# Kernel optimization log

Measured on AMD Instinct MI355X. Metric: run time of the kernel, lower is better.

Reference implementation:

```python
import jax, jax.numpy as jnp
import numpy as np

N_HEADS = 16
NEG_BIG = float(-2**32 + 1)  # value the original writes into masked positions


def setup_inputs() -> dict:
    key = jax.random.key(0)
    ks = jax.random.split(key, 5)
    B, T, D = 64, 256, 1024
    s = 1.0 / np.sqrt(D)
    return {
        "x": jax.random.normal(ks[0], (B, T, D), jnp.float32),
        "pos_emb": jax.random.normal(ks[1], (T, D), jnp.float32),
        "Wq": jax.random.normal(ks[2], (D, D), jnp.float32) * s,
        "Wk": jax.random.normal(ks[3], (D, D), jnp.float32) * s,
        "Wv": jax.random.normal(ks[4], (D, D), jnp.float32) * s,
    }


def reference(x, pos_emb, Wq, Wk, Wv):
    B, T, D = x.shape
    H = N_HEADS
    dh = D // H
    # add position embeddings (same arange positions for every batch row)
    temporal = x + pos_emb[None, :T, :]            # [B, T, D]
    q = temporal @ Wq                              # [B, T, D]
    k = temporal @ Wk
    v = temporal @ Wv
    # chunk along feature dim into H heads, concatenate along batch dim -> [H*B, T, dh]
    def split_heads(t):
        return jnp.concatenate(jnp.split(t, H, axis=2), axis=0)
    q_, k_, v_ = split_heads(q), split_heads(k), split_heads(v)
    scores = jnp.einsum('btd,bsd->bts', q_, k_) / jnp.sqrt(jnp.asarray(T, x.dtype))  # [H*B, T, T]
    # original masks the LOWER triangle (tril > 0 -> padding), faithful to source
    tril = jnp.tril(jnp.ones((T, T), x.dtype))
    scores = jnp.where(tril > 0, jnp.asarray(NEG_BIG, x.dtype), scores)
    # original applies softmax over dim=0 (the batch*head axis), faithful to source
    probs = jax.nn.softmax(scores, axis=0)         # [H*B, T, T]
    out = jnp.einsum('bts,bsd->btd', probs, v_)    # [H*B, T, dh]
    # merge heads back: chunk along batch dim, concatenate along feature dim
    out = jnp.concatenate(jnp.split(out, H, axis=0), axis=-1)  # [B, T, D]
    return out
```

## Files before the change

### kernel.cpp

```cpp
#include <hip/hip_runtime.h>

constexpr int SEQ = 256;
constexpr int DIM = 1024;
constexpr float SCALE = 0.0625f;

typedef __attribute__((ext_vector_type(8))) short bf16x8;
typedef __attribute__((ext_vector_type(4))) float f32x4;
typedef unsigned short ushort_t;
typedef unsigned int uint_t;

__device__ __forceinline__ void gld_lds16(const void* g, void* l) {
  __builtin_amdgcn_global_load_lds(
      (const __attribute__((address_space(1))) unsigned int*)g,
      (__attribute__((address_space(3))) unsigned int*)l, 16, 0, 0);
}

__device__ __forceinline__ ushort_t f2bf(float f) {
  uint_t u = __float_as_uint(f);
  return (ushort_t)((u + 0x7fffu + ((u >> 16) & 1u)) >> 16);
}

__global__ __launch_bounds__(256)
void prep_a(const float* __restrict__ x, const float* __restrict__ pos,
            ushort_t* __restrict__ Ab) {
  const size_t idx = ((size_t)blockIdx.x * 256 + threadIdx.x) * 8;
  const int m = (int)(idx >> 10), k = (int)(idx & 1023);
  float4 x0 = *(const float4*)(x + idx);
  float4 x1 = *(const float4*)(x + idx + 4);
  const float* pp = pos + ((size_t)(m & 255) << 10) + k;
  float4 p0 = *(const float4*)pp;
  float4 p1 = *(const float4*)(pp + 4);
  uint_t w0 = (uint_t)f2bf(x0.x + p0.x) | ((uint_t)f2bf(x0.y + p0.y) << 16);
  uint_t w1 = (uint_t)f2bf(x0.z + p0.z) | ((uint_t)f2bf(x0.w + p0.w) << 16);
  uint_t w2 = (uint_t)f2bf(x1.x + p1.x) | ((uint_t)f2bf(x1.y + p1.y) << 16);
  uint_t w3 = (uint_t)f2bf(x1.z + p1.z) | ((uint_t)f2bf(x1.w + p1.w) << 16);
  *(uint4*)&Ab[idx] = make_uint4(w0, w1, w2, w3);
}

__global__ __launch_bounds__(256)
void pack_w(const float* __restrict__ Wq, const float* __restrict__ Wk,
            const float* __restrict__ Wv, ushort_t* __restrict__ Bp) {
  const float* W = (blockIdx.z == 0) ? Wq : (blockIdx.z == 1) ? Wk : Wv;
  const int n  = blockIdx.x * 256 + threadIdx.x;
  const int k8 = blockIdx.y * 8;
  uint_t h[8];
#pragma unroll
  for (int i = 0; i < 8; ++i) h[i] = f2bf(W[(size_t)(k8 + i) * DIM + n]);
  uint_t hp[4];
#pragma unroll
  for (int j = 0; j < 4; ++j) hp[j] = h[2 * j] | (h[2 * j + 1] << 16);
  const int np = blockIdx.z * 1024 + n;
  const int nb = np >> 7, nl = np & 127;
  const int kc = k8 >> 6, kk = k8 & 63;
  size_t base = (((size_t)nb * 16 + kc) * 128 + nl) * 64 + kk;
  *(uint4*)&Bp[base] = make_uint4(hp[0], hp[1], hp[2], hp[3]);
}

__global__ __launch_bounds__(256)
void qkv_mfma(const ushort_t* __restrict__ Ab, const ushort_t* __restrict__ Bp,
              ushort_t* __restrict__ q_bf, ushort_t* __restrict__ k_bf,
              ushort_t* __restrict__ vT_bf) {
  const int nb = blockIdx.x;
  const int mb = blockIdx.y;
  const int tid = threadIdx.x;
  const int wave = tid >> 6, lane = tid & 63;
  const int wm = wave & 1, wn = wave >> 1;
  const int l15 = lane & 15, quad = lane >> 4;

  __shared__ ushort_t smem[18432];
  ushort_t* As = smem;
  ushort_t* Bs = smem + 8192;

  f32x4 acc[4][4] = {};

  const int sr = lane >> 3;
  const int scg = (lane & 7) ^ (sr & 7);
  const size_t arow = ((size_t)mb * 128 + wave * 32 + sr) * 1024;
  const size_t btile0 = ((size_t)nb * 16) * 128 * 64;

  const int swz = l15 & 7;
  const int a_off0 = (wm * 64 + l15) * 64 + ((quad) ^ swz) * 8;
  const int a_off1 = (wm * 64 + l15) * 64 + ((4 + quad) ^ swz) * 8;
  const int b_off0 = (wn * 64 + l15) * 64 + ((quad) ^ swz) * 8;
  const int b_off1 = (wn * 64 + l15) * 64 + ((4 + quad) ^ swz) * 8;

  for (int kc = 0; kc < 16; ++kc) {
    __syncthreads();
#pragma unroll
    for (int c = 0; c < 4; ++c)
      gld_lds16(Ab + arow + (size_t)c * 8192 + kc * 64 + scg * 8,
                &As[(wave * 32 + c * 8) * 64]);
    const ushort_t* bt = Bp + btile0 + (size_t)kc * 8192;
#pragma unroll
    for (int c = 0; c < 4; ++c)
      gld_lds16(bt + (wave * 32 + c * 8 + sr) * 64 + scg * 8,
                &Bs[(wave * 32 + c * 8) * 64]);
    __syncthreads();

    bf16x8 a0[4], a1[4], b0[4], b1[4];
#pragma unroll
    for (int i = 0; i < 4; ++i) {
      a0[i] = *(const bf16x8*)&As[a_off0 + i * 1024];
      a1[i] = *(const bf16x8*)&As[a_off1 + i * 1024];
    }
#pragma unroll
    for (int j = 0; j < 4; ++j) {
      b0[j] = *(const bf16x8*)&Bs[b_off0 + j * 1024];
      b1[j] = *(const bf16x8*)&Bs[b_off1 + j * 1024];
    }
#pragma unroll
    for (int i = 0; i < 4; ++i)
#pragma unroll
      for (int j = 0; j < 4; ++j) {
        acc[i][j] = __builtin_amdgcn_mfma_f32_16x16x32_bf16(a0[i], b0[j], acc[i][j], 0, 0, 0);
        acc[i][j] = __builtin_amdgcn_mfma_f32_16x16x32_bf16(a1[i], b1[j], acc[i][j], 0, 0, 0);
      }
  }

  const int wq = nb >> 3;
  const int h  = (nb & 7) * 2 + wn;
  const int b  = mb >> 1;
  const int tb0 = (mb & 1) * 128 + wm * 64;
  if (wq < 2) {
    ushort_t* base = ((wq == 0) ? q_bf : k_bf) + (size_t)(b * 16 + h) * SEQ * 64;
    const int tb = tb0 + quad * 4;
#pragma unroll
    for (int i = 0; i < 4; ++i)
#pragma unroll
      for (int j = 0; j < 4; ++j) {
        const int d = l15 + j * 16;
#pragma unroll
        for (int r = 0; r < 4; ++r)
          base[(size_t)(tb + i * 16 + r) * 64 + d] = f2bf(acc[i][j][r]);
      }
  } else {
    __syncthreads();
    ushort_t* L = smem + wave * (64 * 72);
#pragma unroll
    for (int i = 0; i < 4; ++i)
#pragma unroll
      for (int j = 0; j < 4; ++j) {
        uint_t lo = (uint_t)f2bf(acc[i][j][0]) | ((uint_t)f2bf(acc[i][j][1]) << 16);
        uint_t hi = (uint_t)f2bf(acc[i][j][2]) | ((uint_t)f2bf(acc[i][j][3]) << 16);
        *(uint2*)&L[(l15 + j * 16) * 72 + i * 16 + quad * 4] = make_uint2(lo, hi);
      }
    ushort_t* vbase = vT_bf + (size_t)(b * 16 + h) * 64 * SEQ + tb0;
    const int dr = lane >> 3;
    const int tc = (lane & 7) * 8;
#pragma unroll
    for (int u = 0; u < 8; ++u) {
      const int d = u * 8 + dr;
      uint4 val = *(const uint4*)&L[d * 72 + tc];
      *(uint4*)&vbase[(size_t)d * SEQ + tc] = val;
    }
  }
}

__global__ __launch_bounds__(256)
void stats_mfma(const ushort_t* __restrict__ qb, const ushort_t* __restrict__ kb,
                float* __restrict__ part_l) {
  const int p = blockIdx.x, g = blockIdx.y;
  int tt, ss;
  if (p < 4) { tt = p; ss = p; }
  else {
    const int idx = p - 4;
    tt = (idx < 3) ? 0 : (idx < 5) ? 1 : 2;
    ss = (idx < 3) ? idx + 1 : (idx < 5) ? idx - 1 : 3;
  }
  const bool diag = (p < 4);
  const int tid = threadIdx.x, wave = tid >> 6, lane = tid & 63;
  const int l15 = lane & 15, quad = lane >> 4;
  const int slot = g * 4 + wave;

  f32x4 lacc[4][4] = {};

  for (int i4 = 0; i4 < 4; ++i4) {
    const int bp = slot * 4 + i4;
    const int bh = (bp & 63) * 16 + (bp >> 6);
    const ushort_t* qt = qb + (size_t)bh * (SEQ * 64) + (size_t)(tt * 64) * 64;
    const ushort_t* kt = kb + (size_t)bh * (SEQ * 64) + (size_t)(ss * 64) * 64;
    bf16x8 aq[4][2], bk[4][2];
#pragma unroll
    for (int m = 0; m < 4; ++m)
#pragma unroll
      for (int ks = 0; ks < 2; ++ks) {
        aq[m][ks] = *(const bf16x8*)&qt[(m * 16 + l15) * 64 + ks * 32 + quad * 8];
        bk[m][ks] = *(const bf16x8*)&kt[(m * 16 + l15) * 64 + ks * 32 + quad * 8];
      }
    f32x4 sf[4][4] = {};
#pragma unroll
    for (int ks = 0; ks < 2; ++ks)
#pragma unroll
      for (int m = 0; m < 4; ++m)
#pragma unroll
        for (int n = 0; n < 4; ++n)
          sf[m][n] = __builtin_amdgcn_mfma_f32_16x16x32_bf16(aq[m][ks], bk[n][ks], sf[m][n], 0, 0, 0);
#pragma unroll
    for (int m = 0; m < 4; ++m)
#pragma unroll
      for (int n = 0; n < 4; ++n)
#pragma unroll
        for (int r = 0; r < 4; ++r) {
          float e = __expf(sf[m][n][r] * SCALE);
          if (diag) {
            const int t = tt * 64 + m * 16 + quad * 4 + r;
            const int s = ss * 64 + n * 16 + l15;
            e = (s > t) ? e : 1.0f;
          }
          lacc[m][n][r] += e;
        }
  }
  float* pl = part_l + (size_t)slot * (SEQ * SEQ);
#pragma unroll
  for (int m = 0; m < 4; ++m)
#pragma unroll
    for (int r = 0; r < 4; ++r) {
      const int t = tt * 64 + m * 16 + quad * 4 + r;
#pragma unroll
      for (int n = 0; n < 4; ++n)
        pl[(size_t)t * SEQ + ss * 64 + n * 16 + l15] = lacc[m][n][r];
    }
}

__global__ __launch_bounds__(256)
void merge_kernel(const float* __restrict__ part_l, float* __restrict__ inv_lT) {
  const int i = blockIdx.x * 256 + threadIdx.x;
  const int t = i >> 8, s = i & 255;
  float invv;
  if (s <= t) invv = 1.0f / 1024.0f;
  else {
    float sum = 0.f;
    for (int g = 0; g < 256; ++g) sum += part_l[(size_t)g * (SEQ * SEQ) + i];
    invv = 1.0f / sum;
  }
  inv_lT[s * SEQ + t] = invv;
}

__global__ __launch_bounds__(256)
void pv_mfma(const ushort_t* __restrict__ qb, const ushort_t* __restrict__ kb,
             const ushort_t* __restrict__ vtb, const float* __restrict__ inv_lT,
             float* __restrict__ out) {
  const int bh = blockIdx.x;
  const int b = bh >> 4, h = bh & 15;
  const int tid = threadIdx.x, wave = tid >> 6, lane = tid & 63;
  const int l15 = lane & 15, quad = lane >> 4;
  const int t0 = wave * 64;

  __shared__ ushort_t Plds[4][64][72];
  ushort_t (*Pw)[72] = Plds[wave];

  const ushort_t* qq = qb + (size_t)bh * (SEQ * 64);
  const ushort_t* kk = kb + (size_t)bh * (SEQ * 64);
  const ushort_t* vv = vtb + (size_t)bh * (64 * SEQ);

  bf16x8 qf[4][2];
#pragma unroll
  for (int nt = 0; nt < 4; ++nt)
#pragma unroll
    for (int ks = 0; ks < 2; ++ks)
      qf[nt][ks] = *(const bf16x8*)&qq[(t0 + nt * 16 + l15) * 64 + ks * 32 + quad * 8];

  f32x4 o[4][4] = {};

  for (int sc = 0; sc < 4; ++sc) {
    if (sc < wave) {
      const uint_t c = 0x3A803A80u;
      const uint4 cc = make_uint4(c, c, c, c);
#pragma unroll
      for (int u = 0; u < 8; ++u) *(uint4*)&Pw[lane][u * 8] = cc;
    } else {
      bf16x8 kf[4][2];
#pragma unroll
      for (int ms = 0; ms < 4; ++ms)
#pragma unroll
        for (int ks = 0; ks < 2; ++ks)
          kf[ms][ks] = *(const bf16x8*)&kk[(sc * 64 + ms * 16 + l15) * 64 + ks * 32 + quad * 8];
      f32x4 sf[4][4] = {};
#pragma unroll
      for (int ks = 0; ks < 2; ++ks)
#pragma unroll
        for (int ms = 0; ms < 4; ++ms)
#pragma unroll
          for (int nt = 0; nt < 4; ++nt)
            sf[ms][nt] = __builtin_amdgcn_mfma_f32_16x16x32_bf16(kf[ms][ks], qf[nt][ks], sf[ms][nt], 0, 0, 0);
      const bool dg = (sc == wave);
      const int t = t0 + l15;
#pragma unroll
      for (int ms = 0; ms < 4; ++ms)
#pragma unroll
        for (int nt = 0; nt < 4; ++nt) {
          const int sb = sc * 64 + ms * 16 + quad * 4;
          const int tc = t + nt * 16;
          ushort_t pb[4];
#pragma unroll
          for (int r = 0; r < 4; ++r) {
            const int s = sb + r;
            float e = __expf(sf[ms][nt][r] * SCALE);
            if (dg) e = (s > tc) ? e : 1.0f;
            pb[r] = f2bf(e * inv_lT[(size_t)s * SEQ + tc]);
          }
          uint_t lo = (uint_t)pb[0] | ((uint_t)pb[1] << 16);
          uint_t hi = (uint_t)pb[2] | ((uint_t)pb[3] << 16);
          *(uint2*)&Pw[nt * 16 + l15][ms * 16 + quad * 4] = make_uint2(lo, hi);
        }
    }
    bf16x8 vf[4][2], pf[4][2];
#pragma unroll
    for (int nd = 0; nd < 4; ++nd)
#pragma unroll
      for (int ks = 0; ks < 2; ++ks)
        vf[nd][ks] = *(const bf16x8*)&vv[(nd * 16 + l15) * SEQ + sc * 64 + ks * 32 + quad * 8];
#pragma unroll
    for (int mt = 0; mt < 4; ++mt)
#pragma unroll
      for (int ks = 0; ks < 2; ++ks)
        pf[mt][ks] = *(const bf16x8*)&Pw[mt * 16 + l15][ks * 32 + quad * 8];
#pragma unroll
    for (int ks = 0; ks < 2; ++ks)
#pragma unroll
      for (int mt = 0; mt < 4; ++mt)
#pragma unroll
        for (int nd = 0; nd < 4; ++nd)
          o[mt][nd] = __builtin_amdgcn_mfma_f32_16x16x32_bf16(pf[mt][ks], vf[nd][ks], o[mt][nd], 0, 0, 0);
  }

  float* ob = out + (size_t)b * SEQ * DIM + h * 64;
#pragma unroll
  for (int mt = 0; mt < 4; ++mt)
#pragma unroll
    for (int r = 0; r < 4; ++r) {
      const int t = t0 + mt * 16 + quad * 4 + r;
#pragma unroll
      for (int nd = 0; nd < 4; ++nd)
        ob[(size_t)t * DIM + nd * 16 + l15] = o[mt][nd][r];
    }
}

extern "C" void kernel_launch(void* const* d_in, const int* in_sizes, int n_in,
                              void* d_out, int out_size, void* d_ws, size_t ws_size,
                              hipStream_t stream) {
  const float* x   = (const float*)d_in[0];
  const float* pos = (const float*)d_in[1];
  const float* Wq  = (const float*)d_in[2];
  const float* Wk  = (const float*)d_in[3];
  const float* Wv  = (const float*)d_in[4];
  float* out = (float*)d_out;

  ushort_t* Ab = (ushort_t*)d_out;
  ushort_t* Bp = (ushort_t*)((char*)d_out + 33554432);

  char* W = (char*)d_ws;
  ushort_t* q_bf   = (ushort_t*)(W);
  ushort_t* k_bf   = (ushort_t*)(W + 33554432);
  ushort_t* vT_bf  = (ushort_t*)(W + 67108864);
  float*    part_l = (float*)  (W + 100663296);
  float*    inv_lT = (float*)  (W + 167772160);

  prep_a<<<dim3(8192), 256, 0, stream>>>(x, pos, Ab);
  pack_w<<<dim3(4, 128, 3), 256, 0, stream>>>(Wq, Wk, Wv, Bp);
  qkv_mfma<<<dim3(24, 128), 256, 0, stream>>>(Ab, Bp, q_bf, k_bf, vT_bf);
  stats_mfma<<<dim3(10, 64), 256, 0, stream>>>(q_bf, k_bf, part_l);
  merge_kernel<<<dim3(SEQ * SEQ / 256), 256, 0, stream>>>(part_l, inv_lT);
  pv_mfma<<<dim3(1024), 256, 0, stream>>>(q_bf, k_bf, vT_bf, inv_lT, out);
}
```

Before: 374.9 us.

## Enlarge QKV GEMM tiles to 256x256 with double-buffered LDS pipeline

The QKV projection GEMM moves from 128x128 tiles with 4 waves to 256x256 tiles with 8 waves. The K-loop is now software-pipelined, with two LDS buffers, staged global-to-LDS loads interleaved with MFMA phases, explicit vmcnt waits and setprio. The weight packing layout changes to match the 256-wide N tiles. The aim is more data reuse per tile and hiding of load latency behind MFMAs. Separately, the merge kernel's 256-way reduction is split across 8 independent accumulators to raise memory-level parallelism. The risks are higher register pressure and 128KB of LDS per block, which limits occupancy.

```diff
diff --git a/kernel.cpp b/kernel.cpp
--- a/kernel.cpp
+++ b/kernel.cpp
@@ -50,110 +50,141 @@
 #pragma unroll
   for (int j = 0; j < 4; ++j) hp[j] = h[2 * j] | (h[2 * j + 1] << 16);
   const int np = blockIdx.z * 1024 + n;
-  const int nb = np >> 7, nl = np & 127;
+  const int nb = np >> 8, nl = np & 255;
   const int kc = k8 >> 6, kk = k8 & 63;
-  size_t base = (((size_t)nb * 16 + kc) * 128 + nl) * 64 + kk;
+  size_t base = (((size_t)nb * 16 + kc) * 256 + nl) * 64 + kk;
   *(uint4*)&Bp[base] = make_uint4(hp[0], hp[1], hp[2], hp[3]);
 }
 
-__global__ __launch_bounds__(256)
+__global__ __launch_bounds__(512, 2)
 void qkv_mfma(const ushort_t* __restrict__ Ab, const ushort_t* __restrict__ Bp,
               ushort_t* __restrict__ q_bf, ushort_t* __restrict__ k_bf,
               ushort_t* __restrict__ vT_bf) {
   const int nb = blockIdx.x;
   const int mb = blockIdx.y;
-  const int tid = threadIdx.x;
+  const int tid = (int)threadIdx.x;
   const int wave = tid >> 6, lane = tid & 63;
-  const int wm = wave & 1, wn = wave >> 1;
+  const int wm = wave >> 2, wn = wave & 3;
   const int l15 = lane & 15, quad = lane >> 4;
 
-  __shared__ ushort_t smem[18432];
-  ushort_t* As = smem;
-  ushort_t* Bs = smem + 8192;
-
-  f32x4 acc[4][4] = {};
-
-  const int sr = lane >> 3;
-  const int scg = (lane & 7) ^ (sr & 7);
-  const size_t arow = ((size_t)mb * 128 + wave * 32 + sr) * 1024;
-  const size_t btile0 = ((size_t)nb * 16) * 128 * 64;
+  __shared__ ushort_t smem[65536];
+
+  const int r8 = lane >> 3;
+  const int lc8 = ((lane & 7) ^ r8) * 8;
+  const size_t a_row = ((size_t)(mb * 256 + wave * 8 + r8)) << 10;
+  const size_t b_row = ((size_t)((nb * 16) * 256 + wave * 8 + r8)) << 6;
+  const int wb = wave * 512;
+
+#define SA(q, tt, c) gld_lds16(Ab + a_row + ((size_t)(q) << 16) + (size_t)(tt) * 64 + lc8, \
+                               smem + (c) * 32768 + (q) * 4096 + wb)
+#define SB(q, tt, c) gld_lds16(Bp + b_row + (size_t)(tt) * 16384 + (q) * 4096 + lc8, \
+                               smem + (c) * 32768 + 16384 + (q) * 4096 + wb)
 
   const int swz = l15 & 7;
-  const int a_off0 = (wm * 64 + l15) * 64 + ((quad) ^ swz) * 8;
-  const int a_off1 = (wm * 64 + l15) * 64 + ((4 + quad) ^ swz) * 8;
-  const int b_off0 = (wn * 64 + l15) * 64 + ((quad) ^ swz) * 8;
-  const int b_off1 = (wn * 64 + l15) * 64 + ((4 + quad) ^ swz) * 8;
-
-  for (int kc = 0; kc < 16; ++kc) {
-    __syncthreads();
-#pragma unroll
-    for (int c = 0; c < 4; ++c)
-      gld_lds16(Ab + arow + (size_t)c * 8192 + kc * 64 + scg * 8,
-                &As[(wave * 32 + c * 8) * 64]);
-    const ushort_t* bt = Bp + btile0 + (size_t)kc * 8192;
-#pragma unroll
-    for (int c = 0; c < 4; ++c)
-      gld_lds16(bt + (wave * 32 + c * 8 + sr) * 64 + scg * 8,
-                &Bs[(wave * 32 + c * 8) * 64]);
-    __syncthreads();
-
-    bf16x8 a0[4], a1[4], b0[4], b1[4];
-#pragma unroll
-    for (int i = 0; i < 4; ++i) {
-      a0[i] = *(const bf16x8*)&As[a_off0 + i * 1024];
-      a1[i] = *(const bf16x8*)&As[a_off1 + i * 1024];
-    }
-#pragma unroll
-    for (int j = 0; j < 4; ++j) {
-      b0[j] = *(const bf16x8*)&Bs[b_off0 + j * 1024];
-      b1[j] = *(const bf16x8*)&Bs[b_off1 + j * 1024];
-    }
-#pragma unroll
-    for (int i = 0; i < 4; ++i)
+  const int cko0 = (quad ^ swz) * 8;
+  const int cko1 = ((4 + quad) ^ swz) * 8;
+  const int arow0 = (wm * 128 + l15) * 64;
+  const int brow0 = (wn * 64 + l15) * 64;
+
+  f32x4 acc[8][4] = {};
+  bf16x8 a_cur[4][2], b_all[4][2];
+
+#define LDA(IH) do { _Pragma("unroll") for (int ii = 0; ii < 4; ++ii) { \
+    const int ro = arow0 + ((IH) * 64 + ii * 16) * 64; \
+    a_cur[ii][0] = *(const bf16x8*)&Ac[ro + cko0]; \
+    a_cur[ii][1] = *(const bf16x8*)&Ac[ro + cko1]; } } while (0)
+#define LDB(J) do { const int ro = brow0 + (J) * 1024; \
+    b_all[J][0] = *(const bf16x8*)&Bc[ro + cko0]; \
+    b_all[J][1] = *(const bf16x8*)&Bc[ro + cko1]; } while (0)
+#define MM(IH, J0) do { \
+    asm volatile("s_waitcnt lgkmcnt(0)" ::: "memory"); \
+    __builtin_amdgcn_s_setprio(1); \
+    _Pragma("unroll") for (int ks = 0; ks < 2; ++ks) \
+    _Pragma("unroll") for (int ii = 0; ii < 4; ++ii) \
+    _Pragma("unroll") for (int jj = 0; jj < 2; ++jj) \
+      acc[(IH)*4+ii][(J0)+jj] = __builtin_amdgcn_mfma_f32_16x16x32_bf16( \
+          a_cur[ii][ks], b_all[(J0)+jj][ks], acc[(IH)*4+ii][(J0)+jj], 0, 0, 0); \
+    __builtin_amdgcn_s_setprio(0); } while (0)
+
+  SA(0, 0, 0); SA(2, 0, 0); SB(0, 0, 0); SB(1, 0, 0); SB(2, 0, 0); SB(3, 0, 0);
+  SA(1, 0, 0); SA(3, 0, 0);
+  SB(0, 1, 1); SB(1, 1, 1); SA(0, 1, 1); SA(2, 1, 1);
+  asm volatile("s_waitcnt vmcnt(6)" ::: "memory");
+  __builtin_amdgcn_s_barrier();
+
+  for (int t = 0; t < 16; ++t) {
+    const int cur = t & 1, nxt = cur ^ 1;
+    const int tn  = (t < 15) ? t + 1 : 15;
+    const int tn2 = (t < 14) ? t + 2 : 15;
+    const ushort_t* Ac = &smem[cur * 32768];
+    const ushort_t* Bc = Ac + 16384;
+    LDA(0); LDB(0); LDB(1);
+    SB(2, tn, nxt); SB(3, tn, nxt);
+    __builtin_amdgcn_s_barrier();
+    MM(0, 0);
+    __builtin_amdgcn_s_barrier();
+    LDB(2); LDB(3);
+    SA(1, tn, nxt); SA(3, tn, nxt);
+    __builtin_amdgcn_s_barrier();
+    MM(0, 2);
+    asm volatile("s_waitcnt vmcnt(8)" ::: "memory");
+    __builtin_amdgcn_s_barrier();
+    LDA(1);
+    SB(0, tn2, cur); SB(1, tn2, cur);
+    __builtin_amdgcn_s_barrier();
+    MM(1, 2);
+    __builtin_amdgcn_s_barrier();
+    SA(0, tn2, cur); SA(2, tn2, cur);
+    __builtin_amdgcn_s_barrier();
+    MM(1, 0);
+    asm volatile("s_waitcnt vmcnt(6)" ::: "memory");
+    __builtin_amdgcn_s_barrier();
+  }
+
+  asm volatile("s_waitcnt vmcnt(0)" ::: "memory");
+  const int wq = nb >> 2;
+  const int h  = (nb & 3) * 4 + wn;
+  if (wq < 2) {
+    ushort_t* base = ((wq == 0) ? q_bf : k_bf) + (size_t)(mb * 16 + h) * (SEQ * 64);
+    const int tb = wm * 128 + quad * 4;
+#pragma unroll
+    for (int i = 0; i < 8; ++i)
 #pragma unroll
       for (int j = 0; j < 4; ++j) {
-        acc[i][j] = __builtin_amdgcn_mfma_f32_16x16x32_bf16(a0[i], b0[j], acc[i][j], 0, 0, 0);
-        acc[i][j] = __builtin_amdgcn_mfma_f32_16x16x32_bf16(a1[i], b1[j], acc[i][j], 0, 0, 0);
-      }
-  }
-
-  const int wq = nb >> 3;
-  const int h  = (nb & 7) * 2 + wn;
-  const int b  = mb >> 1;
-  const int tb0 = (mb & 1) * 128 + wm * 64;
-  if (wq < 2) {
-    ushort_t* base = ((wq == 0) ? q_bf : k_bf) + (size_t)(b * 16 + h) * SEQ * 64;
-    const int tb = tb0 + quad * 4;
-#pragma unroll
-    for (int i = 0; i < 4; ++i)
-#pragma unroll
-      for (int j = 0; j < 4; ++j) {
-        const int d = l15 + j * 16;
+        const int d = j * 16 + l15;
 #pragma unroll
         for (int r = 0; r < 4; ++r)
           base[(size_t)(tb + i * 16 + r) * 64 + d] = f2bf(acc[i][j][r]);
       }
   } else {
-    __syncthreads();
-    ushort_t* L = smem + wave * (64 * 72);
-#pragma unroll
-    for (int i = 0; i < 4; ++i)
-#pragma unroll
-      for (int j = 0; j < 4; ++j) {
-        uint_t lo = (uint_t)f2bf(acc[i][j][0]) | ((uint_t)f2bf(acc[i][j][1]) << 16);
-        uint_t hi = (uint_t)f2bf(acc[i][j][2]) | ((uint_t)f2bf(acc[i][j][3]) << 16);
-        *(uint2*)&L[(l15 + j * 16) * 72 + i * 16 + quad * 4] = make_uint2(lo, hi);
+    __builtin_amdgcn_s_barrier();
+    ushort_t* L = &smem[wave * 4608];
+    ushort_t* vbase = vT_bf + (size_t)(mb * 16 + h) * (64 * SEQ) + wm * 128;
+    const int tc = (lane & 7) * 8;
+#pragma unroll
+    for (int g = 0; g < 2; ++g) {
+#pragma unroll
+      for (int ii = 0; ii < 4; ++ii)
+#pragma unroll
+        for (int j = 0; j < 4; ++j) {
+          f32x4 v = acc[g * 4 + ii][j];
+          uint_t lo = (uint_t)f2bf(v[0]) | ((uint_t)f2bf(v[1]) << 16);
+          uint_t hi = (uint_t)f2bf(v[2]) | ((uint_t)f2bf(v[3]) << 16);
+          *(uint2*)&L[(j * 16 + l15) * 72 + ii * 16 + quad * 4] = make_uint2(lo, hi);
+        }
+#pragma unroll
+      for (int u = 0; u < 8; ++u) {
+        const int d = u * 8 + r8;
+        uint4 val = *(const uint4*)&L[d * 72 + tc];
+        *(uint4*)&vbase[(size_t)d * SEQ + g * 64 + tc] = val;
       }
-    ushort_t* vbase = vT_bf + (size_t)(b * 16 + h) * 64 * SEQ + tb0;
-    const int dr = lane >> 3;
-    const int tc = (lane & 7) * 8;
-#pragma unroll
-    for (int u = 0; u < 8; ++u) {
-      const int d = u * 8 + dr;
-      uint4 val = *(const uint4*)&L[d * 72 + tc];
-      *(uint4*)&vbase[(size_t)d * SEQ + tc] = val;
     }
   }
+#undef SA
+#undef SB
+#undef LDA
+#undef LDB
+#undef MM
 }
 
 __global__ __launch_bounds__(256)
@@ -229,9 +260,15 @@
   float invv;
   if (s <= t) invv = 1.0f / 1024.0f;
   else {
-    float sum = 0.f;
-    for (int g = 0; g < 256; ++g) sum += part_l[(size_t)g * (SEQ * SEQ) + i];
-    invv = 1.0f / sum;
+    const float* p = part_l + i;
+    float a0 = 0.f, a1 = 0.f, a2 = 0.f, a3 = 0.f,
+          a4 = 0.f, a5 = 0.f, a6 = 0.f, a7 = 0.f;
+    for (int g = 0; g < 256; g += 8) {
+      const float* q = p + ((size_t)g << 16);
+      a0 += q[0ull << 16]; a1 += q[1ull << 16]; a2 += q[2ull << 16]; a3 += q[3ull << 16];
+      a4 += q[4ull << 16]; a5 += q[5ull << 16]; a6 += q[6ull << 16]; a7 += q[7ull << 16];
+    }
+    invv = 1.0f / (((a0 + a1) + (a2 + a3)) + ((a4 + a5) + (a6 + a7)));
   }
   inv_lT[s * SEQ + t] = invv;
 }
@@ -358,7 +395,7 @@
 
   prep_a<<<dim3(8192), 256, 0, stream>>>(x, pos, Ab);
   pack_w<<<dim3(4, 128, 3), 256, 0, stream>>>(Wq, Wk, Wv, Bp);
-  qkv_mfma<<<dim3(24, 128), 256, 0, stream>>>(Ab, Bp, q_bf, k_bf, vT_bf);
+  qkv_mfma<<<dim3(12, 64), 512, 0, stream>>>(Ab, Bp, q_bf, k_bf, vT_bf);
   stats_mfma<<<dim3(10, 64), 256, 0, stream>>>(q_bf, k_bf, part_l);
   merge_kernel<<<dim3(SEQ * SEQ / 256), 256, 0, stream>>>(part_l, inv_lT);
   pv_mfma<<<dim3(1024), 256, 0, stream>>>(q_bf, k_bf, vT_bf, inv_lT, out);
```

New measurement: 366.1 us. -2.4%, faster.
